# Kernel optimization log

Measured on AMD Instinct MI355X. Metric: run time of the kernel, lower is better.

The kernel has to match this reference:

```python
import jax, jax.numpy as jnp
import numpy as np

N_QUBITS = 8
DEPTH = 2
INPUT_DIM = 128
HIDDEN = 128
SEQ = 128
BATCH = 512
DIM = 2 ** N_QUBITS

# Z expectation signs: wire 0 is the most-significant qubit of the state index.
_bits = (np.arange(DIM)[None, :] >> (N_QUBITS - 1 - np.arange(N_QUBITS)[:, None])) & 1
Z_SIGNS = jnp.asarray(1.0 - 2.0 * _bits, dtype=jnp.float32)  # [n_wires, DIM]


def _apply_1q(state, mat, wire):
    """Apply a 2x2 gate on `wire`. mat: [2,2] or batched [bsz,2,2]."""
    bsz = state.shape[0]
    st = state.reshape(bsz, 2 ** wire, 2, -1)
    if mat.ndim == 3:
        out = jnp.einsum('bij,bxjy->bxiy', mat, st)
    else:
        out = jnp.einsum('ij,bxjy->bxiy', mat, st)
    return out.reshape(bsz, DIM)


def _rx_mat(theta):  # theta: [bsz] -> [bsz,2,2] complex
    c = jnp.cos(theta * 0.5).astype(jnp.complex64)
    s = ((-1j) * jnp.sin(theta * 0.5)).astype(jnp.complex64)
    return jnp.stack([jnp.stack([c, s], -1), jnp.stack([s, c], -1)], -2)


def _ry_mat(theta):  # scalar theta -> [2,2] complex
    c = jnp.cos(theta * 0.5)
    s = jnp.sin(theta * 0.5)
    return jnp.stack([jnp.stack([c, -s]), jnp.stack([s, c])]).astype(jnp.complex64)


def _cnot_adj(state, wire):
    """CNOT control=wire, target=wire+1 (adjacent wires)."""
    bsz = state.shape[0]
    st = state.reshape(bsz, 2 ** wire, 4, -1)
    st = st[:, :, jnp.array([0, 1, 3, 2]), :]  # |10>-><|11| swap
    return st.reshape(bsz, DIM)


def _qgate(q_in, params):
    """Variational circuit: RX encoding (first N_QUBITS features of q_in),
    DEPTH x (RY layer + CNOT chain), measure Z on each wire."""
    bsz = q_in.shape[0]
    state = jnp.zeros((bsz, DIM), jnp.complex64).at[:, 0].set(1.0)
    for w in range(N_QUBITS):
        state = _apply_1q(state, _rx_mat(q_in[:, w]), w)
    for d in range(DEPTH):
        for w in range(N_QUBITS):
            state = _apply_1q(state, _ry_mat(params[d, w]), w)
        for w in range(N_QUBITS - 1):
            state = _cnot_adj(state, w)
    probs = state.real ** 2 + state.imag ** 2  # [bsz, DIM]
    return probs @ Z_SIGNS.T  # [bsz, n_wires]


def setup_inputs() -> dict:
    key = jax.random.key(0)
    ks = jax.random.split(key, 16)
    d_in = INPUT_DIM + HIDDEN
    inv = 1.0 / jnp.sqrt(jnp.float32(d_in))
    invq = 1.0 / jnp.sqrt(jnp.float32(N_QUBITS))
    return {
        'inputs': jax.random.normal(ks[0], (SEQ, BATCH, INPUT_DIM), jnp.float32),
        'Wq': jax.random.normal(ks[1], (4 * N_QUBITS, d_in), jnp.float32) * inv,
        'bq': jnp.zeros((4 * N_QUBITS,), jnp.float32),
        'pf': jax.random.normal(ks[2], (DEPTH, N_QUBITS), jnp.float32),
        'pi': jax.random.normal(ks[3], (DEPTH, N_QUBITS), jnp.float32),
        'pg': jax.random.normal(ks[4], (DEPTH, N_QUBITS), jnp.float32),
        'po': jax.random.normal(ks[5], (DEPTH, N_QUBITS), jnp.float32),
        'Wf': jax.random.normal(ks[6], (HIDDEN, N_QUBITS), jnp.float32) * invq,
        'bf': jnp.zeros((HIDDEN,), jnp.float32),
        'Wi': jax.random.normal(ks[7], (HIDDEN, N_QUBITS), jnp.float32) * invq,
        'bi': jnp.zeros((HIDDEN,), jnp.float32),
        'Wg': jax.random.normal(ks[8], (HIDDEN, N_QUBITS), jnp.float32) * invq,
        'bg': jnp.zeros((HIDDEN,), jnp.float32),
        'Wo': jax.random.normal(ks[9], (HIDDEN, N_QUBITS), jnp.float32) * invq,
        'bo': jnp.zeros((HIDDEN,), jnp.float32),
    }


def reference(inputs, Wq, bq, pf, pi, pg, po, Wf, bf, Wi, bi, Wg, bg, Wo, bo):
    bsz = inputs.shape[1]
    h0 = jnp.zeros((bsz, HIDDEN), jnp.float32)
    c0 = jnp.zeros((bsz, HIDDEN), jnp.float32)

    def step(carry, x):
        hx, cx = carry
        combined = jnp.concatenate([x, hx], axis=1)
        q_in = combined @ Wq.T + bq  # [bsz, 4*n_qubits]; only first n_qubits used per gate
        f = jax.nn.sigmoid(_qgate(q_in, pf) @ Wf.T + bf)
        i = jax.nn.sigmoid(_qgate(q_in, pi) @ Wi.T + bi)
        g = jnp.tanh(_qgate(q_in, pg) @ Wg.T + bg)
        o = jax.nn.sigmoid(_qgate(q_in, po) @ Wo.T + bo)
        cx_new = f * cx + i * g
        hx_new = o * jnp.tanh(cx_new)
        return (hx_new, cx_new), hx_new

    (hx, cx), outputs = jax.lax.scan(step, (h0, c0), inputs)
    return outputs, hx, cx
```

## Files before the change

kernel.cpp:

```cpp
#include <hip/hip_runtime.h>

#define SEQ 128
#define BATCH 512
#define IN_DIM 128
#define HID 128

typedef float vf2 __attribute__((ext_vector_type(2)));

__device__ __forceinline__ float rcp_f(float x) { return __builtin_amdgcn_rcpf(x); }
__device__ __forceinline__ float tanh_f(float x) { return 1.0f - 2.0f * rcp_f(__expf(2.0f * x) + 1.0f); }

template <int CTRL>
__device__ __forceinline__ float dpp_add(float s) {
  return s + __int_as_float(__builtin_amdgcn_mov_dpp(__float_as_int(s), CTRL, 0xF, 0xF, true));
}

__device__ __forceinline__ float rdlane(float v, int src) {
  return __int_as_float(__builtin_amdgcn_readlane(__float_as_int(v), src));
}

__device__ __forceinline__ void quarter_bcast(float x, float& r0, float& r1, float& r2, float& r3) {
  unsigned xu = __float_as_uint(x);
  auto pr = __builtin_amdgcn_permlane32_swap(xu, xu, false, false);
#if __has_builtin(__builtin_amdgcn_permlane16_swap)
  auto lo = __builtin_amdgcn_permlane16_swap(pr[0], pr[0], false, false);
  auto hi = __builtin_amdgcn_permlane16_swap(pr[1], pr[1], false, false);
  r0 = __uint_as_float(lo[0]); r1 = __uint_as_float(lo[1]);
  r2 = __uint_as_float(hi[0]); r3 = __uint_as_float(hi[1]);
#else
  unsigned s0 = (unsigned)__builtin_amdgcn_ds_swizzle((int)pr[0], 0x401F);
  unsigned s1 = (unsigned)__builtin_amdgcn_ds_swizzle((int)pr[1], 0x401F);
  const bool qo = (threadIdx.x >> 4) & 1;
  r0 = __uint_as_float(qo ? s0 : pr[0]);
  r1 = __uint_as_float(qo ? pr[0] : s0);
  r2 = __uint_as_float(qo ? s1 : pr[1]);
  r3 = __uint_as_float(qo ? pr[1] : s1);
#endif
}

__global__ __launch_bounds__(64) void qlstm_kernel(
    const float* __restrict__ X, const float* __restrict__ Wq, const float* __restrict__ bq,
    const float* __restrict__ pf, const float* __restrict__ pi_, const float* __restrict__ pg,
    const float* __restrict__ po, const float* __restrict__ Wf, const float* __restrict__ bf,
    const float* __restrict__ Wi, const float* __restrict__ bi, const float* __restrict__ Wg,
    const float* __restrict__ bg, const float* __restrict__ Wo, const float* __restrict__ bo,
    float* __restrict__ out)
{
  const int lane = threadIdx.x;
  const int G = lane >> 4;
  const int p = lane & 15;
  const int b = blockIdx.x;

  const float* gW = (G == 0) ? Wf : (G == 1) ? Wi : (G == 2) ? Wg : Wo;
  const float* gB = (G == 0) ? bf : (G == 1) ? bi : (G == 2) ? bg : bo;
  const float* gP = (G == 0) ? pf : (G == 1) ? pi_ : (G == 2) ? pg : po;

  vf2 wxE[4], wxO[4], whE[4], whO[4];
  {
    const vf2* pa = (const vf2*)(Wq + (2 * G) * 256 + 8 * p);
    const vf2* pbh = (const vf2*)(Wq + (2 * G) * 256 + 128 + 8 * p);
    const vf2* pc = (const vf2*)(Wq + (2 * G + 1) * 256 + 8 * p);
    const vf2* pdh = (const vf2*)(Wq + (2 * G + 1) * 256 + 128 + 8 * p);
#pragma unroll
    for (int j = 0; j < 4; ++j) { wxE[j] = pa[j]; whE[j] = pbh[j]; wxO[j] = pc[j]; whO[j] = pdh[j]; }
  }
  const float bqv = bq[2 * G + (p >> 3)];

  vf2 wg2[8][4];
#pragma unroll
  for (int w = 0; w < 8; ++w)
#pragma unroll
    for (int j = 0; j < 4; ++j) {
      wg2[w][j].x = gW[(8 * p + 2 * j) * 8 + w];
      wg2[w][j].y = gW[(8 * p + 2 * j + 1) * 8 + w];
    }
  vf2 bias2[4];
#pragma unroll
  for (int j = 0; j < 4; ++j) {
    bias2[j].x = gB[8 * p + 2 * j];
    bias2[j].y = gB[8 * p + 2 * j + 1];
  }
  vf2 cbsb[8];
  float C1[8], S1[8];
#pragma unroll
  for (int w = 0; w < 8; ++w) {
    float th0 = gP[w], th1 = gP[8 + w];
    cbsb[w].x = cosf(th0); cbsb[w].y = sinf(th0);
    C1[w] = cosf(th1); S1[w] = sinf(th1);
  }
  const float amul = (G == 2) ? 2.0f : 1.0f;
  const float oadd = (G == 2) ? -1.0f : 0.0f;

  float c8[8], h8[8];
#pragma unroll
  for (int k = 0; k < 8; ++k) { c8[k] = 0.0f; h8[k] = 0.0f; }

  const float* xp = X + (size_t)b * IN_DIM + 8 * p;
  float* outp = out + (size_t)b * HID + 8 * p;

  float4 xa, xb, xa2 = {0, 0, 0, 0}, xb2 = {0, 0, 0, 0};
  xa = *(const float4*)(xp);
  xb = *(const float4*)(xp + 4);

#define QSTEP(XA, XB, XAN, XBN, T, PREF)                                         \
  {                                                                              \
    if (PREF) {                                                                  \
      const float* xn_ = xp + (size_t)((T) + 1) * (BATCH * IN_DIM);              \
      XAN = *(const float4*)(xn_);                                               \
      XBN = *(const float4*)(xn_ + 4);                                           \
    }                                                                            \
    vf2 x0_ = {XA.x, XA.y}, x1_ = {XA.z, XA.w};                                  \
    vf2 x2_ = {XB.x, XB.y}, x3_ = {XB.z, XB.w};                                  \
    vf2 h0_ = {h8[0], h8[1]}, h1_ = {h8[2], h8[3]};                              \
    vf2 h2_ = {h8[4], h8[5]}, h3_ = {h8[6], h8[7]};                              \
    vf2 pe_ = wxE[0] * x0_ + wxE[1] * x1_ + wxE[2] * x2_ + wxE[3] * x3_          \
            + whE[0] * h0_ + whE[1] * h1_ + whE[2] * h2_ + whE[3] * h3_;         \
    vf2 po_ = wxO[0] * x0_ + wxO[1] * x1_ + wxO[2] * x2_ + wxO[3] * x3_          \
            + whO[0] * h0_ + whO[1] * h1_ + whO[2] * h2_ + whO[3] * h3_;         \
    float sE_ = pe_.x + pe_.y, sO_ = po_.x + po_.y;                              \
    sE_ = dpp_add<0xB1>(sE_);  sO_ = dpp_add<0xB1>(sO_);                         \
    sE_ = dpp_add<0x4E>(sE_);  sO_ = dpp_add<0x4E>(sO_);                         \
    sE_ = dpp_add<0x141>(sE_); sO_ = dpp_add<0x141>(sO_);                        \
    sE_ = dpp_add<0x140>(sE_); sO_ = dpp_add<0x140>(sO_);                        \
    float z_ = ((p & 8) ? sO_ : sE_) + bqv;                                      \
    float sz_, cz_;                                                              \
    __sincosf(z_, &sz_, &cz_);                                                   \
    float cqs[8], sqs[8];                                                        \
    _Pragma("unroll")                                                            \
    for (int w = 0; w < 8; ++w) {                                                \
      const int src = 16 * (w >> 1) + 8 * (w & 1);                               \
      cqs[w] = rdlane(cz_, src);                                                 \
      sqs[w] = rdlane(sz_, src);                                                 \
    }                                                                            \
    vf2 acc0 = bias2[0], acc1 = bias2[1], acc2 = bias2[2], acc3 = bias2[3];      \
    float u_, d_, P_, R_;                                                        \
    {                                                                            \
      vf2 KA0 = cbsb[0] * cqs[0];                                                \
      u_ = C1[0]; d_ = C1[0] * KA0.x;                                            \
      P_ = -S1[0] * KA0.y; R_ = -S1[0] * sqs[0];                                 \
    }                                                                            \
    _Pragma("unroll")                                                            \
    for (int w = 1; w < 8; ++w) {                                                \
      vf2 KA = cbsb[w] * cqs[w];                                                 \
      float K_ = KA.x, A2_ = KA.y, B2_ = sqs[w];                                 \
      float Md = fmaf(A2_, P_, d_);                                              \
      float MP = fmaf(A2_, d_, P_);                                              \
      float Mu = fmaf(K_, u_, -(B2_ * R_));                                      \
      float MR = fmaf(B2_, u_, K_ * R_);                                         \
      acc0 += Md * wg2[w - 1][0]; acc1 += Md * wg2[w - 1][1];                    \
      acc2 += Md * wg2[w - 1][2]; acc3 += Md * wg2[w - 1][3];                    \
      u_ = C1[w] * Md; d_ = C1[w] * Mu;                                          \
      P_ = -S1[w] * MP; R_ = -S1[w] * MR;                                        \
    }                                                                            \
    float ev7_ = d_ + P_;                                                        \
    acc0 += ev7_ * wg2[7][0]; acc1 += ev7_ * wg2[7][1];                          \
    acc2 += ev7_ * wg2[7][2]; acc3 += ev7_ * wg2[7][3];                          \
    float av_[8] = {acc0.x, acc0.y, acc1.x, acc1.y, acc2.x, acc2.y, acc3.x, acc3.y}; \
    _Pragma("unroll")                                                            \
    for (int k = 0; k < 8; ++k) {                                                \
      float e_ = __expf(-amul * av_[k]);                                         \
      float ok_ = fmaf(rcp_f(1.0f + e_), amul, oadd);                            \
      float Fv_, Iv_, Gg_, Ov_;                                                  \
      quarter_bcast(ok_, Fv_, Iv_, Gg_, Ov_);                                    \
      float cv_ = fmaf(Fv_, c8[k], Iv_ * Gg_);                                   \
      c8[k] = cv_;                                                               \
      h8[k] = Ov_ * tanh_f(cv_);                                                 \
    }                                                                            \
    if (G == 0) {                                                                \
      float* op_ = outp + (size_t)(T) * (BATCH * HID);                           \
      float4 s0_, s1_;                                                           \
      s0_.x = h8[0]; s0_.y = h8[1]; s0_.z = h8[2]; s0_.w = h8[3];                \
      s1_.x = h8[4]; s1_.y = h8[5]; s1_.z = h8[6]; s1_.w = h8[7];                \
      *(float4*)(op_) = s0_;                                                     \
      *(float4*)(op_ + 4) = s1_;                                                 \
    }                                                                            \
  }

#pragma unroll 1
  for (int tt = 0; tt < SEQ; tt += 2) {
    QSTEP(xa, xb, xa2, xb2, tt, true);
    QSTEP(xa2, xb2, xa, xb, tt + 1, (tt + 2 < SEQ));
  }
#undef QSTEP

  if (G == 0) {
    size_t base = (size_t)SEQ * BATCH * HID;
    float* hp = out + base + (size_t)b * HID + 8 * p;
    float* cp = out + base + (size_t)BATCH * HID + (size_t)b * HID + 8 * p;
    float4 v0, v1;
    v0.x = h8[0]; v0.y = h8[1]; v0.z = h8[2]; v0.w = h8[3];
    v1.x = h8[4]; v1.y = h8[5]; v1.z = h8[6]; v1.w = h8[7];
    *(float4*)(hp) = v0; *(float4*)(hp + 4) = v1;
    v0.x = c8[0]; v0.y = c8[1]; v0.z = c8[2]; v0.w = c8[3];
    v1.x = c8[4]; v1.y = c8[5]; v1.z = c8[6]; v1.w = c8[7];
    *(float4*)(cp) = v0; *(float4*)(cp + 4) = v1;
  }
}

extern "C" void kernel_launch(void* const* d_in, const int* in_sizes, int n_in,
                              void* d_out, int out_size, void* d_ws, size_t ws_size,
                              hipStream_t stream) {
  (void)in_sizes; (void)n_in; (void)out_size; (void)d_ws; (void)ws_size;
  const float* X   = (const float*)d_in[0];
  const float* Wq  = (const float*)d_in[1];
  const float* bq  = (const float*)d_in[2];
  const float* pf  = (const float*)d_in[3];
  const float* pi_ = (const float*)d_in[4];
  const float* pg  = (const float*)d_in[5];
  const float* po  = (const float*)d_in[6];
  const float* Wf  = (const float*)d_in[7];
  const float* bf  = (const float*)d_in[8];
  const float* Wi  = (const float*)d_in[9];
  const float* bi  = (const float*)d_in[10];
  const float* Wg  = (const float*)d_in[11];
  const float* bg  = (const float*)d_in[12];
  const float* Wo  = (const float*)d_in[13];
  const float* bo  = (const float*)d_in[14];
  float* out = (float*)d_out;

  qlstm_kernel<<<BATCH, 64, 0, stream>>>(X, Wq, bq, pf, pi_, pg, po,
                                         Wf, bf, Wi, bi, Wg, bg, Wo, bo, out);
}
```

Baseline: 216.3 us.

## Split each batch row across four wavefronts, one per gate, with LDS exchange

Each block now runs 256 threads: one wavefront per LSTM gate, and each lane owns two hidden units instead of eight. The q_in projection is recomputed in every wave with 8-lane groups per qubit, and the hidden state is shared through LDS. Gate activations are also exchanged through LDS with two barriers per timestep, replacing the in-wave permlane broadcasts. This cuts the serial per-lane work on the recurrence critical path, at the cost of barrier and LDS latency every step and duplicated projection work across the four waves.

```diff
diff --git a/kernel.cpp b/kernel.cpp
--- a/kernel.cpp
+++ b/kernel.cpp
@@ -14,31 +14,13 @@
 __device__ __forceinline__ float dpp_add(float s) {
   return s + __int_as_float(__builtin_amdgcn_mov_dpp(__float_as_int(s), CTRL, 0xF, 0xF, true));
 }
-
 __device__ __forceinline__ float rdlane(float v, int src) {
   return __int_as_float(__builtin_amdgcn_readlane(__float_as_int(v), src));
 }
 
-__device__ __forceinline__ void quarter_bcast(float x, float& r0, float& r1, float& r2, float& r3) {
-  unsigned xu = __float_as_uint(x);
-  auto pr = __builtin_amdgcn_permlane32_swap(xu, xu, false, false);
-#if __has_builtin(__builtin_amdgcn_permlane16_swap)
-  auto lo = __builtin_amdgcn_permlane16_swap(pr[0], pr[0], false, false);
-  auto hi = __builtin_amdgcn_permlane16_swap(pr[1], pr[1], false, false);
-  r0 = __uint_as_float(lo[0]); r1 = __uint_as_float(lo[1]);
-  r2 = __uint_as_float(hi[0]); r3 = __uint_as_float(hi[1]);
-#else
-  unsigned s0 = (unsigned)__builtin_amdgcn_ds_swizzle((int)pr[0], 0x401F);
-  unsigned s1 = (unsigned)__builtin_amdgcn_ds_swizzle((int)pr[1], 0x401F);
-  const bool qo = (threadIdx.x >> 4) & 1;
-  r0 = __uint_as_float(qo ? s0 : pr[0]);
-  r1 = __uint_as_float(qo ? pr[0] : s0);
-  r2 = __uint_as_float(qo ? s1 : pr[1]);
-  r3 = __uint_as_float(qo ? pr[1] : s1);
-#endif
-}
+#define BARRIER() asm volatile("s_waitcnt lgkmcnt(0)\n\ts_barrier" ::: "memory")
 
-__global__ __launch_bounds__(64) void qlstm_kernel(
+__global__ __launch_bounds__(256) void qlstm_kernel(
     const float* __restrict__ X, const float* __restrict__ Wq, const float* __restrict__ bq,
     const float* __restrict__ pf, const float* __restrict__ pi_, const float* __restrict__ pg,
     const float* __restrict__ po, const float* __restrict__ Wf, const float* __restrict__ bf,
@@ -46,154 +28,144 @@
     const float* __restrict__ bg, const float* __restrict__ Wo, const float* __restrict__ bo,
     float* __restrict__ out)
 {
-  const int lane = threadIdx.x;
-  const int G = lane >> 4;
-  const int p = lane & 15;
-  const int b = blockIdx.x;
+  __shared__ __align__(16) float gsh[4 * HID];
+  __shared__ __align__(16) float hsw[HID];
 
-  const float* gW = (G == 0) ? Wf : (G == 1) ? Wi : (G == 2) ? Wg : Wo;
-  const float* gB = (G == 0) ? bf : (G == 1) ? bi : (G == 2) ? bg : bo;
-  const float* gP = (G == 0) ? pf : (G == 1) ? pi_ : (G == 2) ? pg : po;
+  const int tid  = threadIdx.x;
+  const int g    = tid >> 6;
+  const int lane = tid & 63;
+  const int r    = lane >> 3;
+  const int c    = lane & 7;
+  const int b    = blockIdx.x;
 
-  vf2 wxE[4], wxO[4], whE[4], whO[4];
+  const float* gW = (g == 0) ? Wf : (g == 1) ? Wi : (g == 2) ? Wg : Wo;
+  const float* gB = (g == 0) ? bf : (g == 1) ? bi : (g == 2) ? bg : bo;
+  const float* gP = (g == 0) ? pf : (g == 1) ? pi_ : (g == 2) ? pg : po;
+
+  vf2 wx[8], wh[8];
   {
-    const vf2* pa = (const vf2*)(Wq + (2 * G) * 256 + 8 * p);
-    const vf2* pbh = (const vf2*)(Wq + (2 * G) * 256 + 128 + 8 * p);
-    const vf2* pc = (const vf2*)(Wq + (2 * G + 1) * 256 + 8 * p);
-    const vf2* pdh = (const vf2*)(Wq + (2 * G + 1) * 256 + 128 + 8 * p);
+    const vf2* pxw = (const vf2*)(Wq + r * 256 + 16 * c);
+    const vf2* phw = (const vf2*)(Wq + r * 256 + 128 + 16 * c);
 #pragma unroll
-    for (int j = 0; j < 4; ++j) { wxE[j] = pa[j]; whE[j] = pbh[j]; wxO[j] = pc[j]; whO[j] = pdh[j]; }
+    for (int j = 0; j < 8; ++j) { wx[j] = pxw[j]; wh[j] = phw[j]; }
   }
-  const float bqv = bq[2 * G + (p >> 3)];
+  const float bqv = bq[r];
 
-  vf2 wg2[8][4];
+  const float amul = (g == 2) ? 2.0f : 1.0f;
+  const float oadd = (g == 2) ? -1.0f : 0.0f;
+  const float ksc  = -amul;
+
+  const int d0 = 2 * lane;
+  vf2 wg2[8];
 #pragma unroll
-  for (int w = 0; w < 8; ++w)
-#pragma unroll
-    for (int j = 0; j < 4; ++j) {
-      wg2[w][j].x = gW[(8 * p + 2 * j) * 8 + w];
-      wg2[w][j].y = gW[(8 * p + 2 * j + 1) * 8 + w];
-    }
-  vf2 bias2[4];
-#pragma unroll
-  for (int j = 0; j < 4; ++j) {
-    bias2[j].x = gB[8 * p + 2 * j];
-    bias2[j].y = gB[8 * p + 2 * j + 1];
+  for (int w = 0; w < 8; ++w) {
+    wg2[w].x = gW[d0 * 8 + w] * ksc;
+    wg2[w].y = gW[(d0 + 1) * 8 + w] * ksc;
   }
-  vf2 cbsb[8];
-  float C1[8], S1[8];
+  vf2 bias2; bias2.x = gB[d0] * ksc; bias2.y = gB[d0 + 1] * ksc;
+
+  vf2 cbsb[8]; float C1[8], S1[8];
 #pragma unroll
   for (int w = 0; w < 8; ++w) {
     float th0 = gP[w], th1 = gP[8 + w];
     cbsb[w].x = cosf(th0); cbsb[w].y = sinf(th0);
     C1[w] = cosf(th1); S1[w] = sinf(th1);
   }
-  const float amul = (G == 2) ? 2.0f : 1.0f;
-  const float oadd = (G == 2) ? -1.0f : 0.0f;
 
-  float c8[8], h8[8];
-#pragma unroll
-  for (int k = 0; k < 8; ++k) { c8[k] = 0.0f; h8[k] = 0.0f; }
+  float* hw_w = (float*)((char*)hsw + (16 * r + 128 * (c >> 1) + 8 * (c & 1)));
+  const float4* hw_r = (const float4*)((char*)hsw + 16 * c);
 
-  const float* xp = X + (size_t)b * IN_DIM + 8 * p;
-  float* outp = out + (size_t)b * HID + 8 * p;
+  float c0r = 0.f, c1r = 0.f, h0v = 0.f, h1v = 0.f;
+  if (g == 3) { vf2 z2; z2.x = 0.f; z2.y = 0.f; *(vf2*)hw_w = z2; }
+  __syncthreads();
 
-  float4 xa, xb, xa2 = {0, 0, 0, 0}, xb2 = {0, 0, 0, 0};
-  xa = *(const float4*)(xp);
-  xb = *(const float4*)(xp + 4);
+  const float* xp = X + (size_t)b * IN_DIM + 16 * c;
+  float* outp = out + (size_t)b * HID + d0;
 
-#define QSTEP(XA, XB, XAN, XBN, T, PREF)                                         \
-  {                                                                              \
-    if (PREF) {                                                                  \
-      const float* xn_ = xp + (size_t)((T) + 1) * (BATCH * IN_DIM);              \
-      XAN = *(const float4*)(xn_);                                               \
-      XBN = *(const float4*)(xn_ + 4);                                           \
-    }                                                                            \
-    vf2 x0_ = {XA.x, XA.y}, x1_ = {XA.z, XA.w};                                  \
-    vf2 x2_ = {XB.x, XB.y}, x3_ = {XB.z, XB.w};                                  \
-    vf2 h0_ = {h8[0], h8[1]}, h1_ = {h8[2], h8[3]};                              \
-    vf2 h2_ = {h8[4], h8[5]}, h3_ = {h8[6], h8[7]};                              \
-    vf2 pe_ = wxE[0] * x0_ + wxE[1] * x1_ + wxE[2] * x2_ + wxE[3] * x3_          \
-            + whE[0] * h0_ + whE[1] * h1_ + whE[2] * h2_ + whE[3] * h3_;         \
-    vf2 po_ = wxO[0] * x0_ + wxO[1] * x1_ + wxO[2] * x2_ + wxO[3] * x3_          \
-            + whO[0] * h0_ + whO[1] * h1_ + whO[2] * h2_ + whO[3] * h3_;         \
-    float sE_ = pe_.x + pe_.y, sO_ = po_.x + po_.y;                              \
-    sE_ = dpp_add<0xB1>(sE_);  sO_ = dpp_add<0xB1>(sO_);                         \
-    sE_ = dpp_add<0x4E>(sE_);  sO_ = dpp_add<0x4E>(sO_);                         \
-    sE_ = dpp_add<0x141>(sE_); sO_ = dpp_add<0x141>(sO_);                        \
-    sE_ = dpp_add<0x140>(sE_); sO_ = dpp_add<0x140>(sO_);                        \
-    float z_ = ((p & 8) ? sO_ : sE_) + bqv;                                      \
-    float sz_, cz_;                                                              \
-    __sincosf(z_, &sz_, &cz_);                                                   \
-    float cqs[8], sqs[8];                                                        \
-    _Pragma("unroll")                                                            \
-    for (int w = 0; w < 8; ++w) {                                                \
-      const int src = 16 * (w >> 1) + 8 * (w & 1);                               \
-      cqs[w] = rdlane(cz_, src);                                                 \
-      sqs[w] = rdlane(sz_, src);                                                 \
-    }                                                                            \
-    vf2 acc0 = bias2[0], acc1 = bias2[1], acc2 = bias2[2], acc3 = bias2[3];      \
-    float u_, d_, P_, R_;                                                        \
-    {                                                                            \
-      vf2 KA0 = cbsb[0] * cqs[0];                                                \
-      u_ = C1[0]; d_ = C1[0] * KA0.x;                                            \
-      P_ = -S1[0] * KA0.y; R_ = -S1[0] * sqs[0];                                 \
-    }                                                                            \
-    _Pragma("unroll")                                                            \
-    for (int w = 1; w < 8; ++w) {                                                \
-      vf2 KA = cbsb[w] * cqs[w];                                                 \
-      float K_ = KA.x, A2_ = KA.y, B2_ = sqs[w];                                 \
-      float Md = fmaf(A2_, P_, d_);                                              \
-      float MP = fmaf(A2_, d_, P_);                                              \
-      float Mu = fmaf(K_, u_, -(B2_ * R_));                                      \
-      float MR = fmaf(B2_, u_, K_ * R_);                                         \
-      acc0 += Md * wg2[w - 1][0]; acc1 += Md * wg2[w - 1][1];                    \
-      acc2 += Md * wg2[w - 1][2]; acc3 += Md * wg2[w - 1][3];                    \
-      u_ = C1[w] * Md; d_ = C1[w] * Mu;                                          \
-      P_ = -S1[w] * MP; R_ = -S1[w] * MR;                                        \
-    }                                                                            \
-    float ev7_ = d_ + P_;                                                        \
-    acc0 += ev7_ * wg2[7][0]; acc1 += ev7_ * wg2[7][1];                          \
-    acc2 += ev7_ * wg2[7][2]; acc3 += ev7_ * wg2[7][3];                          \
-    float av_[8] = {acc0.x, acc0.y, acc1.x, acc1.y, acc2.x, acc2.y, acc3.x, acc3.y}; \
-    _Pragma("unroll")                                                            \
-    for (int k = 0; k < 8; ++k) {                                                \
-      float e_ = __expf(-amul * av_[k]);                                         \
-      float ok_ = fmaf(rcp_f(1.0f + e_), amul, oadd);                            \
-      float Fv_, Iv_, Gg_, Ov_;                                                  \
-      quarter_bcast(ok_, Fv_, Iv_, Gg_, Ov_);                                    \
-      float cv_ = fmaf(Fv_, c8[k], Iv_ * Gg_);                                   \
-      c8[k] = cv_;                                                               \
-      h8[k] = Ov_ * tanh_f(cv_);                                                 \
-    }                                                                            \
-    if (G == 0) {                                                                \
-      float* op_ = outp + (size_t)(T) * (BATCH * HID);                           \
-      float4 s0_, s1_;                                                           \
-      s0_.x = h8[0]; s0_.y = h8[1]; s0_.z = h8[2]; s0_.w = h8[3];                \
-      s1_.x = h8[4]; s1_.y = h8[5]; s1_.z = h8[6]; s1_.w = h8[7];                \
-      *(float4*)(op_) = s0_;                                                     \
-      *(float4*)(op_ + 4) = s1_;                                                 \
-    }                                                                            \
+  float4 xA0, xA1, xA2, xA3, xB0, xB1, xB2, xB3;
+  {
+    const float4* p4 = (const float4*)xp;
+    xA0 = p4[0]; xA1 = p4[1]; xA2 = p4[2]; xA3 = p4[3];
+    xB0 = xA0; xB1 = xA1; xB2 = xA2; xB3 = xA3;
+  }
+
+#define QSTEP(Xc0, Xc1, Xc2, Xc3, Xn0, Xn1, Xn2, Xn3, T, PREF)                        \
+  {                                                                                   \
+    if (PREF) {                                                                       \
+      const float4* xn_ = (const float4*)(xp + (size_t)((T) + 1) * (BATCH * IN_DIM)); \
+      Xn0 = xn_[0]; Xn1 = xn_[1]; Xn2 = xn_[2]; Xn3 = xn_[3];                         \
+    }                                                                                 \
+    float4 hh0 = hw_r[0], hh1 = hw_r[8], hh2 = hw_r[16], hh3 = hw_r[24];              \
+    vf2 aq = wx[0] * (vf2){Xc0.x, Xc0.y} + wx[1] * (vf2){Xc0.z, Xc0.w}                \
+           + wx[2] * (vf2){Xc1.x, Xc1.y} + wx[3] * (vf2){Xc1.z, Xc1.w}                \
+           + wx[4] * (vf2){Xc2.x, Xc2.y} + wx[5] * (vf2){Xc2.z, Xc2.w}                \
+           + wx[6] * (vf2){Xc3.x, Xc3.y} + wx[7] * (vf2){Xc3.z, Xc3.w}                \
+           + wh[0] * (vf2){hh0.x, hh0.y} + wh[1] * (vf2){hh0.z, hh0.w}                \
+           + wh[2] * (vf2){hh1.x, hh1.y} + wh[3] * (vf2){hh1.z, hh1.w}                \
+           + wh[4] * (vf2){hh2.x, hh2.y} + wh[5] * (vf2){hh2.z, hh2.w}                \
+           + wh[6] * (vf2){hh3.x, hh3.y} + wh[7] * (vf2){hh3.z, hh3.w};               \
+    float s_ = aq.x + aq.y;                                                           \
+    s_ = dpp_add<0xB1>(s_); s_ = dpp_add<0x4E>(s_); s_ = dpp_add<0x141>(s_);          \
+    float z_ = s_ + bqv;                                                              \
+    float sz_, cz_;                                                                   \
+    __sincosf(z_, &sz_, &cz_);                                                        \
+    float cqs[8], sqs[8];                                                             \
+    _Pragma("unroll")                                                                 \
+    for (int w = 0; w < 8; ++w) { cqs[w] = rdlane(cz_, 8 * w); sqs[w] = rdlane(sz_, 8 * w); } \
+    vf2 acc = bias2;                                                                  \
+    float u_, d_, P_, R_;                                                             \
+    {                                                                                 \
+      vf2 KA0 = cbsb[0] * cqs[0];                                                     \
+      u_ = C1[0]; d_ = C1[0] * KA0.x;                                                 \
+      P_ = -S1[0] * KA0.y; R_ = -S1[0] * sqs[0];                                      \
+    }                                                                                 \
+    _Pragma("unroll")                                                                 \
+    for (int w = 1; w < 8; ++w) {                                                     \
+      vf2 KA = cbsb[w] * cqs[w];                                                      \
+      float K_ = KA.x, A2_ = KA.y, B2_ = sqs[w];                                      \
+      float Md = fmaf(A2_, P_, d_);                                                   \
+      float MP = fmaf(A2_, d_, P_);                                                   \
+      float Mu = fmaf(K_, u_, -(B2_ * R_));                                           \
+      float MR = fmaf(B2_, u_, K_ * R_);                                              \
+      acc += Md * wg2[w - 1];                                                         \
+      u_ = C1[w] * Md; d_ = C1[w] * Mu;                                               \
+      P_ = -S1[w] * MP; R_ = -S1[w] * MR;                                             \
+    }                                                                                 \
+    float ev7_ = d_ + P_;                                                             \
+    acc += ev7_ * wg2[7];                                                             \
+    float e0_ = __expf(acc.x), e1_ = __expf(acc.y);                                   \
+    vf2 ok_;                                                                          \
+    ok_.x = fmaf(rcp_f(1.0f + e0_), amul, oadd);                                      \
+    ok_.y = fmaf(rcp_f(1.0f + e1_), amul, oadd);                                      \
+    *(vf2*)(gsh + g * HID + d0) = ok_;                                                \
+    BARRIER();                                                                        \
+    vf2 fv = *(const vf2*)(gsh + 0 * HID + d0);                                       \
+    vf2 iv = *(const vf2*)(gsh + 1 * HID + d0);                                       \
+    vf2 gv = *(const vf2*)(gsh + 2 * HID + d0);                                       \
+    vf2 ov = *(const vf2*)(gsh + 3 * HID + d0);                                       \
+    c0r = fmaf(fv.x, c0r, iv.x * gv.x);                                               \
+    c1r = fmaf(fv.y, c1r, iv.y * gv.y);                                               \
+    h0v = ov.x * tanh_f(c0r);                                                         \
+    h1v = ov.y * tanh_f(c1r);                                                         \
+    if (g == 3) { vf2 hw2; hw2.x = h0v; hw2.y = h1v; *(vf2*)hw_w = hw2; }             \
+    if (g == 0) { vf2 o2; o2.x = h0v; o2.y = h1v;                                     \
+      *(vf2*)(outp + (size_t)(T) * (BATCH * HID)) = o2; }                             \
+    BARRIER();                                                                        \
   }
 
 #pragma unroll 1
   for (int tt = 0; tt < SEQ; tt += 2) {
-    QSTEP(xa, xb, xa2, xb2, tt, true);
-    QSTEP(xa2, xb2, xa, xb, tt + 1, (tt + 2 < SEQ));
+    QSTEP(xA0, xA1, xA2, xA3, xB0, xB1, xB2, xB3, tt, true);
+    QSTEP(xB0, xB1, xB2, xB3, xA0, xA1, xA2, xA3, tt + 1, (tt + 2 < SEQ));
   }
 #undef QSTEP
 
-  if (G == 0) {
+  if (g == 0) {
     size_t base = (size_t)SEQ * BATCH * HID;
-    float* hp = out + base + (size_t)b * HID + 8 * p;
-    float* cp = out + base + (size_t)BATCH * HID + (size_t)b * HID + 8 * p;
-    float4 v0, v1;
-    v0.x = h8[0]; v0.y = h8[1]; v0.z = h8[2]; v0.w = h8[3];
-    v1.x = h8[4]; v1.y = h8[5]; v1.z = h8[6]; v1.w = h8[7];
-    *(float4*)(hp) = v0; *(float4*)(hp + 4) = v1;
-    v0.x = c8[0]; v0.y = c8[1]; v0.z = c8[2]; v0.w = c8[3];
-    v1.x = c8[4]; v1.y = c8[5]; v1.z = c8[6]; v1.w = c8[7];
-    *(float4*)(cp) = v0; *(float4*)(cp + 4) = v1;
+    vf2 hv; hv.x = h0v; hv.y = h1v;
+    vf2 cv; cv.x = c0r; cv.y = c1r;
+    *(vf2*)(out + base + (size_t)b * HID + d0) = hv;
+    *(vf2*)(out + base + (size_t)BATCH * HID + (size_t)b * HID + d0) = cv;
   }
 }
 
@@ -218,6 +190,6 @@
   const float* bo  = (const float*)d_in[14];
   float* out = (float*)d_out;
 
-  qlstm_kernel<<<BATCH, 64, 0, stream>>>(X, Wq, bq, pf, pi_, pg, po,
-                                         Wf, bf, Wi, bi, Wg, bg, Wo, bo, out);
+  qlstm_kernel<<<BATCH, 256, 0, stream>>>(X, Wq, bq, pf, pi_, pg, po,
+                                          Wf, bf, Wi, bi, Wg, bg, Wo, bo, out);
 }
```

After: 231.8 us. 7.1% more time.
